# Kernel optimization log

Hardware: AMD Instinct MI355X
Metric: run time of the kernel (lower is better)

## Reference

```python
import jax, jax.numpy as jnp
import numpy as np
from math import factorial

# ---- configuration (init_kwargs: nclasses=40, cfg.bw=16) ----
BW = 16            # spherical bandwidth
NB = 2 * BW        # grid samples per angle
M = 2 * BW - 1     # spectral orders m in [-(BW-1), BW-1]
OFF = BW - 1       # index offset: m -> m + OFF
NCLS = 40
EPS = 1e-5
BATCH = 8

_FACT = [float(factorial(i)) for i in range(4 * BW + 2)]

def _wigner_d(l, beta):
    """Wigner small-d matrix d^l_{m',m}(beta), shape [2l+1, 2l+1]."""
    c, s = np.cos(beta / 2.0), np.sin(beta / 2.0)
    d = np.zeros((2 * l + 1, 2 * l + 1))
    for imp, mp in enumerate(range(-l, l + 1)):
        for im, m in enumerate(range(-l, l + 1)):
            pref = np.sqrt(_FACT[l + mp] * _FACT[l - mp] * _FACT[l + m] * _FACT[l - m])
            acc = 0.0
            for k in range(max(0, m - mp), min(l + m, l - mp) + 1):
                acc += ((-1.0) ** (mp - m + k)
                        / (_FACT[l + m - k] * _FACT[k] * _FACT[l - k - mp] * _FACT[k - m + mp])
                        * c ** (2 * l - 2 * k + m - mp) * s ** (2 * k - m + mp))
            d[imp, im] = pref * acc
    return d

def _build_constants():
    # Driscoll-Healy beta quadrature grid and weights
    betas = np.pi * (2 * np.arange(NB) + 1) / (4 * BW)
    kk = np.arange(BW)
    qw = (2.0 / BW) * np.sin(betas) * (
        np.sin(np.outer(2 * np.arange(NB) + 1, 2 * kk + 1) * np.pi / (4 * BW)) @ (1.0 / (2 * kk + 1)))
    d_beta = np.zeros((NB, BW, M, M))      # d^l_{mn}(beta_j), zero-padded over l
    for j, beta in enumerate(betas):
        for l in range(BW):
            d_beta[j, l, OFF - l:OFF + l + 1, OFF - l:OFF + l + 1] = _wigner_d(l, beta)
    d_eq = np.zeros((BW, M, M))            # d^l_{mn}(pi/2) for the equatorial kernel grid
    for l in range(BW):
        d_eq[l, OFF - l:OFF + l + 1, OFF - l:OFF + l + 1] = _wigner_d(l, np.pi / 2)
    bins = (np.arange(-(BW - 1), BW) % NB).astype(np.int32)  # FFT bin for each order m
    return qw.astype(np.float32), d_beta.astype(np.float32), d_eq.astype(np.float32), bins

_QWn, _DBETAn, _DEQn, _BINSn = _build_constants()
_DBJ = jnp.asarray(_DBETAn)                                   # [NB, L, M, M]
_DEQJ = jnp.asarray(_DEQn)                                    # [L, M, M]
_DEQ0 = jnp.asarray(_DEQn[:, :, OFF])                         # [L, M]  (n = 0 column)
_WD_S2 = jnp.asarray(_QWn[:, None, None] * _DBETAn[:, :, :, OFF])   # [NB, L, M]
_WD_SO3 = jnp.asarray(_QWn[:, None, None, None] * _DBETAn)          # [NB, L, M, M]
_L2 = jnp.asarray((2.0 * np.arange(BW) + 1.0).astype(np.float32))
_BINSJ = jnp.asarray(_BINSn)

def _so3_ifft(z, bias):
    # z: [B, Co, L, M, M] SO(3) spectrum -> real signal [B, Co, NB(beta), NB(alpha), NB(gamma)]
    F = jnp.einsum('bolmn,jlmn,l->bojmn', z, _DBJ, _L2)
    grid = jnp.zeros(F.shape[:3] + (NB, NB), F.dtype)
    grid = grid.at[..., _BINSJ[:, None], _BINSJ[None, :]].set(F)
    sig = jnp.fft.ifft2(grid, axes=(-2, -1)).real * float(NB * NB)
    return sig + bias[None, :, None, None, None]

def _s2_conv(x, W, bias):
    # x: [B, Ci, NB(beta), NB(alpha)]; W: [Ci, Co, NB] kernel on the equatorial grid
    Xf = jnp.fft.fft(x, axis=-1)[..., _BINSJ]                 # [B,Ci,NB,M]
    xh = jnp.einsum('bcjm,jlm->bclm', Xf, _WD_S2)             # S2 FFT -> [B,Ci,L,M]
    Wf = jnp.fft.fft(W, axis=-1)[..., _BINSJ]                 # [Ci,Co,M]
    yh = _DEQ0[:, :, None, None] * jnp.transpose(Wf, (2, 0, 1))[None]   # [L,N,Ci,Co]
    z = jnp.einsum('bilm,lnio->bolmn', xh, jnp.conj(yh))      # S2 correlation -> SO(3) spectrum
    return _so3_ifft(z, bias)

def _so3_conv(x, W, bias):
    # x: [B, Ci, NB(beta), NB(alpha), NB(gamma)]; W: [Ci, Co, NB]
    Xf = jnp.fft.fft2(x, axes=(-2, -1))[..., _BINSJ[:, None], _BINSJ[None, :]]  # [B,Ci,NB,M,M]
    xh = jnp.einsum('bcjmn,jlmn->bclmn', Xf, _WD_SO3)         # SO(3) FFT -> [B,Ci,L,M,M]
    Wf = jnp.fft.fft(W, axis=-1)[..., _BINSJ]                 # [Ci,Co,M]
    yh = _DEQJ[:, :, :, None, None] * jnp.transpose(Wf, (2, 0, 1))[None, :, None]  # [L,N,K,Ci,Co]
    z = jnp.einsum('bilmk,lnkio->bolmn', xh, jnp.conj(yh))    # SO(3) correlation
    return _so3_ifft(z, bias)

def _bn(h, g, b, axes, shape):
    mu = jnp.mean(h, axes, keepdims=True)
    var = jnp.var(h, axes, keepdims=True)
    return (h - mu) * jax.lax.rsqrt(var + EPS) * g.reshape(shape) + b.reshape(shape)

def _forward(x, k1, c1b, bn1_g, bn1_b, k2, c2b, bn2_g, bn2_b, k3, c3b, bn3_g, bn3_b,
             fc1_w, fc1_b, fbn1_g, fbn1_b, fc2_w, fc2_b, fbn2_g, fbn2_b, fc3_w, fc3_b):
    s5 = (1, -1, 1, 1, 1)
    h = _s2_conv(x, k1, c1b)                                  # [B,50,NB,NB,NB]
    h = jax.nn.relu(_bn(h, bn1_g, bn1_b, (0, 2, 3, 4), s5))
    h = _so3_conv(h, k2, c2b)
    h = jax.nn.relu(_bn(h, bn2_g, bn2_b, (0, 2, 3, 4), s5))
    h = _so3_conv(h, k3, c3b)
    h = jax.nn.relu(_bn(h, bn3_g, bn3_b, (0, 2, 3, 4), s5))
    h = h.mean(-1)                                            # integrate over gamma
    h = h.reshape(h.shape[0], h.shape[1], -1).max(-1)         # global max pool -> [B,50]
    h = h @ fc1_w.T + fc1_b
    h = jax.nn.relu(_bn(h, fbn1_g, fbn1_b, (0,), (1, -1)))
    h = h @ fc2_w.T + fc2_b
    h = jax.nn.relu(_bn(h, fbn2_g, fbn2_b, (0,), (1, -1)))
    h = h @ fc3_w.T + fc3_b
    return jax.nn.log_softmax(h, axis=1)

def setup_inputs():
    key = jax.random.key(0)
    ks = jax.random.split(key, 24)
    f32 = jnp.float32
    def kern(k, ci, co):
        return jax.random.normal(k, (ci, co, NB), f32) / np.sqrt(ci * NB).astype(np.float32)
    def lin(k, co, ci):
        return jax.random.normal(k, (co, ci), f32) / np.sqrt(ci).astype(np.float32)
    return {
        'x': jax.random.normal(ks[0], (BATCH, 1, NB, NB), f32),
        'k1': kern(ks[1], 1, 50), 'c1b': 0.01 * jax.random.normal(ks[2], (50,), f32),
        'bn1_g': 1.0 + 0.1 * jax.random.normal(ks[3], (50,), f32),
        'bn1_b': 0.1 * jax.random.normal(ks[4], (50,), f32),
        'k2': kern(ks[5], 50, 50), 'c2b': 0.01 * jax.random.normal(ks[6], (50,), f32),
        'bn2_g': 1.0 + 0.1 * jax.random.normal(ks[7], (50,), f32),
        'bn2_b': 0.1 * jax.random.normal(ks[8], (50,), f32),
        'k3': kern(ks[9], 50, 50), 'c3b': 0.01 * jax.random.normal(ks[10], (50,), f32),
        'bn3_g': 1.0 + 0.1 * jax.random.normal(ks[11], (50,), f32),
        'bn3_b': 0.1 * jax.random.normal(ks[12], (50,), f32),
        'fc1_w': lin(ks[13], 256, 50), 'fc1_b': jnp.zeros((256,), f32),
        'fbn1_g': 1.0 + 0.1 * jax.random.normal(ks[14], (256,), f32),
        'fbn1_b': 0.1 * jax.random.normal(ks[15], (256,), f32),
        'fc2_w': lin(ks[16], 128, 256), 'fc2_b': jnp.zeros((128,), f32),
        'fbn2_g': 1.0 + 0.1 * jax.random.normal(ks[17], (128,), f32),
        'fbn2_b': 0.1 * jax.random.normal(ks[18], (128,), f32),
        'fc3_w': lin(ks[19], NCLS, 128), 'fc3_b': jnp.zeros((NCLS,), f32),
    }

def reference(x, k1, c1b, bn1_g, bn1_b, k2, c2b, bn2_g, bn2_b, k3, c3b, bn3_g, bn3_b,
              fc1_w, fc1_b, fbn1_g, fbn1_b, fc2_w, fc2_b, fbn2_g, fbn2_b, fc3_w, fc3_b):
    return _forward(x, k1, c1b, bn1_g, bn1_b, k2, c2b, bn2_g, bn2_b, k3, c3b, bn3_g, bn3_b,
                    fc1_w, fc1_b, fbn1_g, fbn1_b, fc2_w, fc2_b, fbn2_g, fbn2_b, fc3_w, fc3_b)
```

## Files before the change

### kernel.cpp

```cpp
#include <hip/hip_runtime.h>
#include <math.h>

constexpr int NB = 32;
constexpr int LL = 16;
constexpr int MM = 31;
constexpr int MOFF = 15;
constexpr int NBATCH = 8;
constexpr int NCH = 50;
constexpr int NQ = MM * MM;
constexpr int SPAT = NB * NB * NB;
constexpr long long HN = (long long)NBATCH * NCH * SPAT;

#define PI_D 3.14159265358979323846

__device__ inline float2 c_mk(float x, float y) { float2 r; r.x = x; r.y = y; return r; }

__device__ inline void fill_tw(float2* tw) {
  int t = threadIdx.x;
  if (t < 32) {
    double a = (double)t * (PI_D / 16.0);
    tw[t] = c_mk((float)cos(a), (float)sin(a));
  }
}

__device__ inline int bitrev5(int n) {
  return ((n & 1) << 4) | ((n & 2) << 2) | (n & 4) | ((n & 8) >> 2) | ((n & 16) >> 4);
}

__device__ inline double dpow(double x, int n) {
  double r = 1.0;
  for (int i = 0; i < n; ++i) r *= x;
  return r;
}


__global__ void qw_kernel(float* __restrict__ qw) {
  int j = threadIdx.x;
  if (j >= NB) return;
  double beta = PI_D * (2 * j + 1) / 64.0;
  double acc = 0.0;
  for (int kk = 0; kk < LL; ++kk)
    acc += sin((double)(2 * j + 1) * (2 * kk + 1) * PI_D / 64.0) / (double)(2 * kk + 1);
  qw[j] = (float)((2.0 / 16.0) * sin(beta) * acc);
}

__global__ void wigner_kernel(float* __restrict__ out, int nj, int eqmode) {
  __shared__ double fact[66];
  int tid = threadIdx.x;
  if (tid < 66) { double f = 1.0; for (int i = 2; i <= tid; ++i) f *= (double)i; fact[tid] = f; }
  __syncthreads();
  int total = nj * LL * NQ;
  int idx = blockIdx.x * blockDim.x + tid;
  if (idx >= total) return;
  int q = idx % NQ;
  int l = (idx / NQ) % LL;
  int j = idx / (NQ * LL);
  int mp = q / MM - MOFF;
  int m  = q % MM - MOFF;
  int amp = mp < 0 ? -mp : mp, am = m < 0 ? -m : m;
  float res = 0.f;
  if (amp <= l && am <= l) {
    double beta = eqmode ? (PI_D * 0.5) : (PI_D * (2 * j + 1) / 64.0);
    double c = cos(beta * 0.5), s = sin(beta * 0.5);
    double pref = sqrt(fact[l + mp] * fact[l - mp] * fact[l + m] * fact[l - m]);
    int k0 = max(0, m - mp), k1 = min(l + m, l - mp);
    double acc = 0.0;
    for (int k = k0; k <= k1; ++k) {
      double denom = fact[l + m - k] * fact[k] * fact[l - k - mp] * fact[k - m + mp];
      double term = dpow(c, 2 * l - 2 * k + m - mp) * dpow(s, 2 * k - m + mp) / denom;
      acc += ((mp - m + k) & 1) ? -term : term;
    }
    res = (float)(pref * acc);
  }
  out[idx] = res;
}

__global__ void transpose_d_kernel(const float* __restrict__ dbeta, float* __restrict__ dbT) {
  int idx = blockIdx.x * blockDim.x + threadIdx.x;
  if (idx >= NB * LL * NQ) return;
  int m = idx % MM;
  int n = (idx / MM) % MM;
  int jl = idx / NQ;
  dbT[idx] = dbeta[jl * NQ + m * MM + n];
}


__global__ __launch_bounds__(256) void s2_xh_kernel(const float* __restrict__ x,
                                                    const float* __restrict__ qw,
                                                    const float* __restrict__ dbeta,
                                                    float2* __restrict__ xh1) {
  __shared__ float xt[NB * NB];
  __shared__ float2 Xf0[NB * MM];
  __shared__ float2 tw[32];
  fill_tw(tw);
  int tid = threadIdx.x, b = blockIdx.x;
  for (int e = tid; e < NB * NB; e += 256) xt[e] = x[b * 1024 + e];
  __syncthreads();
  for (int e = tid; e < NB * MM; e += 256) {
    int j = e / MM, mi = e % MM, m = mi - MOFF;
    float re = 0.f, im = 0.f;
    const float* row = xt + j * NB;
    for (int a = 0; a < NB; ++a) {
      float v = row[a];
      float2 t = tw[(m * a) & 31];
      re += v * t.x; im -= v * t.y;
    }
    Xf0[e] = c_mk(re, im);
  }
  __syncthreads();
  for (int e = tid; e < LL * MM; e += 256) {
    int l = e / MM, mi = e % MM;
    float re = 0.f, im = 0.f;
    for (int j = 0; j < NB; ++j) {
      float w = qw[j] * dbeta[(j * LL + l) * NQ + mi * MM + MOFF];
      float2 X = Xf0[j * MM + mi];
      re += w * X.x; im += w * X.y;
    }
    xh1[(b * LL + l) * MM + mi] = c_mk(re, im);
  }
}

__global__ __launch_bounds__(256) void wfft_kernel(const float* __restrict__ W, int CiCo,
                                                   float2* __restrict__ Wf) {
  __shared__ float2 tw[32];
  fill_tw(tw);
  __syncthreads();
  int idx = blockIdx.x * blockDim.x + threadIdx.x;
  if (idx >= MM * CiCo) return;
  int ni = idx / CiCo, ic = idx % CiCo;
  int n = ni - MOFF;
  float re = 0.f, im = 0.f;
  for (int t = 0; t < NB; ++t) {
    float v = W[ic * NB + t];
    float2 tt = tw[(n * t) & 31];
    re += v * tt.x; im -= v * tt.y;
  }
  Wf[idx] = c_mk(re, im);
}

__global__ void s2_z_kernel(const float2* __restrict__ xh1, const float2* __restrict__ Wf1,
                            const float* __restrict__ deq, float2* __restrict__ z) {
  int idx = blockIdx.x * blockDim.x + threadIdx.x;
  if (idx >= NBATCH * NCH * LL * NQ) return;
  int mi = idx % MM; int t = idx / MM;
  int ni = t % MM; t /= MM;
  int l = t % LL; t /= LL;
  int o = t % NCH; int b = t / NCH;
  float d0 = deq[(l * MM + ni) * MM + MOFF];
  float2 xv = xh1[(b * LL + l) * MM + mi];
  float2 wv = Wf1[ni * NCH + o];
  float re = d0 * (xv.x * wv.x + xv.y * wv.y);
  float im = d0 * (xv.y * wv.x - xv.x * wv.y);
  z[idx] = c_mk(re, im);
}


__global__ __launch_bounds__(256) void fjq_kernel(const float2* __restrict__ z,
                                                  const float* __restrict__ dbT,
                                                  float2* __restrict__ F) {
  __shared__ float2 zs[2][LL][8];
  int qg = blockIdx.x % 121;
  int bg = blockIdx.x / 121;
  int tid = threadIdx.x;
  int j = tid >> 3, ql = tid & 7;
  int q = qg * 8 + ql;
  bool qok = q < NQ;
  int qc = qok ? q : NQ - 1;
  float w[LL];
  #pragma unroll
  for (int l = 0; l < LL; ++l)
    w[l] = (2.f * l + 1.f) * dbT[(j * LL + l) * NQ + qc];
  int bo0 = bg * 25;
  if (tid < 128) {
    int l = tid >> 3, qq = qg * 8 + (tid & 7);
    int dd = (qq < NQ) ? (qq / MM - MOFF) : 99; if (dd < 0) dd = -dd;
    zs[0][l][tid & 7] = (l >= dd) ? z[((long long)bo0 * LL + l) * NQ + qq] : c_mk(0.f, 0.f);
  }
  __syncthreads();
  for (int i = 0; i < 25; ++i) {
    int bo = bo0 + i;
    if (i < 24 && tid < 128) {
      int l = tid >> 3, qq = qg * 8 + (tid & 7);
      int dd = (qq < NQ) ? (qq / MM - MOFF) : 99; if (dd < 0) dd = -dd;
      zs[(i + 1) & 1][l][tid & 7] =
          (l >= dd) ? z[((long long)(bo + 1) * LL + l) * NQ + qq] : c_mk(0.f, 0.f);
    }
    float fr = 0.f, fi = 0.f;
    #pragma unroll
    for (int l = 0; l < LL; ++l) {
      float2 zv = zs[i & 1][l][ql];
      fr += w[l] * zv.x; fi += w[l] * zv.y;
    }
    if (qok) F[((long long)bo * NB + j) * NQ + q] = c_mk(fr, fi);
    __syncthreads();
  }
}

__global__ __launch_bounds__(64) void so3_dft_kernel(const float2* __restrict__ F,
                                                     const float* __restrict__ bias,
                                                     float* __restrict__ out,
                                                     float2* __restrict__ parts) {
  __shared__ float Sre[2][32][33];
  __shared__ float Sim[2][32][33];
  __shared__ float2 tw[32];
  fill_tw(tw);
  int tid = threadIdx.x;
  int lane = tid & 31;
  int t = tid >> 5;
  int idx = blockIdx.x * 2 + t;
  int j = idx & 31;
  int bo = idx >> 5;
  int o = bo % NCH;

  Sre[t][16][lane] = 0.f; Sim[t][16][lane] = 0.f;
  Sre[t][lane][16] = 0.f; Sim[t][lane][16] = 0.f;
  __syncthreads();

  const float2* src = F + ((long long)bo * NB + j) * NQ;
  for (int e = lane; e < NQ; e += 32) {
    int ni = e / MM, mi = e % MM;
    float2 v = src[e];
    Sre[t][(ni + 17) & 31][(mi + 17) & 31] = v.x;
    Sim[t][(ni + 17) & 31][(mi + 17) & 31] = v.y;
  }
  __syncthreads();

  float vr[32], vi[32];

  #pragma unroll
  for (int r = 0; r < 32; ++r) { vr[r] = Sre[t][r][lane]; vi[r] = Sim[t][r][lane]; }
  #pragma unroll
  for (int st = 0; st < 5; ++st) {
    const int half = 16 >> st, tmul = 1 << st;
    #pragma unroll
    for (int p = 0; p < 16; ++p) {
      const int j2 = p & (half - 1);
      const int i0 = ((p >> (4 - st)) << (5 - st)) + j2;
      const int i1 = i0 + half;
      float2 tt = tw[(j2 * tmul) & 31];
      float ur = vr[i0], ui = vi[i0], wr = vr[i1], wi = vi[i1];
      float dr = ur - wr, di = ui - wi;
      vr[i0] = ur + wr; vi[i0] = ui + wi;
      vr[i1] = dr * tt.x - di * tt.y;
      vi[i1] = dr * tt.y + di * tt.x;
    }
  }
  #pragma unroll
  for (int k = 0; k < 32; ++k) {
    Sre[t][k][lane] = vr[bitrev5(k)];
    Sim[t][k][lane] = vi[bitrev5(k)];
  }
  __syncthreads();

  #pragma unroll
  for (int m = 0; m < 32; ++m) { vr[m] = Sre[t][lane][m]; vi[m] = Sim[t][lane][m]; }
  #pragma unroll
  for (int st = 0; st < 5; ++st) {
    const int half = 16 >> st, tmul = 1 << st;
    #pragma unroll
    for (int p = 0; p < 16; ++p) {
      const int j2 = p & (half - 1);
      const int i0 = ((p >> (4 - st)) << (5 - st)) + j2;
      const int i1 = i0 + half;
      float2 tt = tw[(j2 * tmul) & 31];
      float ur = vr[i0], ui = vi[i0], wr = vr[i1], wi = vi[i1];
      float dr = ur - wr, di = ui - wi;
      vr[i0] = ur + wr; vi[i0] = ui + wi;
      vr[i1] = dr * tt.x - di * tt.y;
      vi[i1] = dr * tt.y + di * tt.x;
    }
  }

  float bval = bias[o];
  long long obase = (long long)bo * SPAT + (long long)j * 1024 + lane;
  float s1 = 0.f, s2 = 0.f;
  #pragma unroll
  for (int a = 0; a < 32; ++a) {
    float val = vr[bitrev5(a)] + bval;
    out[obase + a * 32] = val;
    s1 += val; s2 += val * val;
  }
  #pragma unroll
  for (int off = 32; off > 0; off >>= 1) {
    s1 += __shfl_down(s1, off);
    s2 += __shfl_down(s2, off);
  }
  if (tid == 0) {
    atomicAdd(&parts[bo].x, s1);
    atomicAdd(&parts[bo].y, s2);
  }
}


__global__ void bn_finalize_kernel(const float2* __restrict__ partials,
                                   const float* __restrict__ g, const float* __restrict__ bb,
                                   float2* __restrict__ sc) {
  int o = threadIdx.x;
  if (o >= NCH) return;
  float s = 0.f, ss = 0.f;
  for (int b = 0; b < NBATCH; ++b) { float2 p = partials[b * NCH + o]; s += p.x; ss += p.y; }
  float inv = 1.f / (float)(NBATCH * SPAT);
  float mu = s * inv;
  float var = ss * inv - mu * mu;
  float scale = g[o] * rsqrtf(var + 1e-5f);
  sc[o] = c_mk(scale, bb[o] - mu * scale);
}


__global__ __launch_bounds__(256) void dft2b_kernel(const float* __restrict__ h,
                                                    const float2* __restrict__ sc,
                                                    float2* __restrict__ Xf) {
  __shared__ float xt[32 * 33];
  __shared__ float2 P[32 * 16];
  __shared__ float2 Xs[NQ];
  __shared__ float2 tw[32];
  fill_tw(tw);
  int tid = threadIdx.x;
  long long blk = blockIdx.x;
  int c = (int)((blk >> 5) % NCH);
  float2 s = sc[c];
  const float* src = h + blk * 1024;
  for (int e = tid; e < 1024; e += 256) {
    float v = src[e];
    xt[(e >> 5) * 33 + (e & 31)] = fmaxf(v * s.x + s.y, 0.f);
  }
  __syncthreads();
  for (int e = tid; e < 512; e += 256) {
    int a = e >> 4, n = e & 15;
    float re = 0.f, im = 0.f;
    const float* row = xt + a * 33;
    #pragma unroll
    for (int g = 0; g < 32; ++g) {
      float v = row[g];
      float2 t = tw[(n * g) & 31];
      re += v * t.x; im -= v * t.y;
    }
    P[a * 16 + n] = c_mk(re, im);
  }
  __syncthreads();
  {
    int e = tid;
    if (e < 256) {
      int mh = e >> 4, n = e & 15;
      float sxx = 0.f, sxy = 0.f, syx = 0.f, syy = 0.f;
      #pragma unroll
      for (int a = 0; a < 32; ++a) {
        float2 p = P[a * 16 + n];
        float2 t = tw[(mh * a) & 31];
        sxx += p.x * t.x; sxy += p.x * t.y;
        syx += p.y * t.x; syy += p.y * t.y;
      }
      float2 Xp = c_mk(sxx + syy, syx - sxy);
      float2 Xm = c_mk(sxx - syy, syx + sxy);
      Xs[(mh + MOFF) * MM + (n + MOFF)] = Xp;
      Xs[(MOFF - mh) * MM + (n + MOFF)] = Xm;
      Xs[(MOFF - mh) * MM + (MOFF - n)] = c_mk(Xp.x, -Xp.y);
      Xs[(mh + MOFF) * MM + (MOFF - n)] = c_mk(Xm.x, -Xm.y);
    }
  }
  __syncthreads();
  float2* dst = Xf + blk * NQ;
  for (int e = tid; e < NQ; e += 256) dst[e] = Xs[e];
}

__global__ void xh_kernel(const float2* __restrict__ Xf, const float* __restrict__ qw,
                          const float* __restrict__ dbeta, float2* __restrict__ xh) {
  int idx = blockIdx.x * blockDim.x + threadIdx.x;
  if (idx >= NBATCH * NCH * NQ) return;
  int q = idx % NQ;
  int bc = idx / NQ;
  int dm = q / MM - MOFF; if (dm < 0) dm = -dm;
  int dn = q % MM - MOFF; if (dn < 0) dn = -dn;
  int lmin = dm > dn ? dm : dn;
  float2 acc[LL];
  #pragma unroll
  for (int l = 0; l < LL; ++l) acc[l] = c_mk(0.f, 0.f);
  for (int j = 0; j < NB; ++j) {
    float2 xv = Xf[((long long)bc * NB + j) * NQ + q];
    float qj = qw[j];
    const float* dbase = dbeta + (long long)(j * LL) * NQ + q;
    #pragma unroll
    for (int l = 0; l < LL; ++l) {
      float w = qj * dbase[l * NQ];
      acc[l].x += w * xv.x;
      acc[l].y += w * xv.y;
    }
  }
  #pragma unroll
  for (int l = 0; l < LL; ++l)
    if (l >= lmin) xh[((long long)bc * LL + l) * NQ + q] = acc[l];
}

__global__ __launch_bounds__(64) void hk_kernel(const float2* __restrict__ xh,
                                                const float* __restrict__ deq,
                                                float2* __restrict__ hk2) {
  int r = blockIdx.x;
  int mi = r % MM;
  int lb = r / MM;
  int b = lb & 7;
  int l = lb >> 3;
  int adm = mi - MOFF; adm = adm < 0 ? -adm : adm;
  if (adm > l) return;
  int ich = threadIdx.x;
  if (ich >= NCH) return;
  float2 row[MM];
  const float2* src = xh + ((long long)(b * NCH + ich) * LL + l) * NQ + mi * MM;
  #pragma unroll
  for (int k = 0; k < MM; ++k) row[k] = src[k];
  const float* dl = deq + l * NQ;
  long long obase = (long long)r * MM * NCH + ich;
  for (int ni = MOFF - l; ni <= MOFF + l; ++ni) {
    const float* dr = dl + ni * MM;
    float re = 0.f, im = 0.f;
    #pragma unroll
    for (int k = 0; k < MM; ++k) {
      float d = dr[k];
      re += d * row[k].x;
      im += d * row[k].y;
    }
    hk2[obase + (long long)ni * NCH] = c_mk(re, im);
  }
}

__global__ __launch_bounds__(256) void z_kernel(const float2* __restrict__ hk2,
                                                const float2* __restrict__ Wf,
                                                float2* __restrict__ z) {
  __shared__ float2 ws[NCH * NCH];
  int blk = blockIdx.x;
  int ni = 0;
  for (;;) {
    int d = ni - MOFF; if (d < 0) d = -d;
    int nt = 32 - 2 * d;
    if (blk < nt) break;
    blk -= nt; ++ni;
  }
  int dmin = ni - MOFF; if (dmin < 0) dmin = -dmin;
  int tid = threadIdx.x;
  {
    const float4* s4 = reinterpret_cast<const float4*>(Wf + ni * (NCH * NCH));
    float4* d4 = reinterpret_cast<float4*>(ws);
    for (int e = tid; e < NCH * NCH / 2; e += 256) d4[e] = s4[e];
  }
  __syncthreads();
  if (tid >= 248) return;
  int r = dmin * 248 + blk * 124 + (tid % 124);
  int o0 = (tid / 124) * 25;
  int mi = r % MM;
  int rem = r / MM;
  int b = rem & 7;
  int l = rem >> 3;

  const float4* h4 = reinterpret_cast<const float4*>(hk2 + ((long long)r * MM + ni) * NCH);

  float2 acc[25];
  #pragma unroll
  for (int u = 0; u < 25; ++u) acc[u] = c_mk(0.f, 0.f);

  for (int ih = 0; ih < 25; ++ih) {
    float4 hv = h4[ih];
    const float2* w0 = ws + (2 * ih) * NCH + o0;
    #pragma unroll
    for (int u = 0; u < 25; ++u) {
      float2 w = w0[u];
      acc[u].x += hv.x * w.x + hv.y * w.y;
      acc[u].y += hv.y * w.x - hv.x * w.y;
    }
    const float2* w1 = w0 + NCH;
    #pragma unroll
    for (int u = 0; u < 25; ++u) {
      float2 w = w1[u];
      acc[u].x += hv.z * w.x + hv.w * w.y;
      acc[u].y += hv.w * w.x - hv.z * w.y;
    }
  }

  long long zbase = (((long long)(b * NCH + o0) * LL + l) * NQ) + ni * MM + mi;
  #pragma unroll
  for (int u = 0; u < 25; ++u)
    z[zbase + (long long)u * LL * NQ] = acc[u];
}


__global__ void pool_kernel(const float* __restrict__ h, const float2* __restrict__ sc,
                            float* __restrict__ pooled) {
  __shared__ float sm[256];
  int tid = threadIdx.x;
  int o = blockIdx.x % NCH;
  float2 s = sc[o];
  const float* base = h + (long long)blockIdx.x * SPAT;
  float best = -1e30f;
  for (int e = tid; e < 1024; e += 256) {
    float acc = 0.f;
    for (int g = 0; g < NB; ++g) {
      float v = base[e * NB + g];
      acc += fmaxf(v * s.x + s.y, 0.f);
    }
    best = fmaxf(best, acc * (1.f / 32.f));
  }
  sm[tid] = best;
  __syncthreads();
  for (int st = 128; st > 0; st >>= 1) {
    if (tid < st) sm[tid] = fmaxf(sm[tid], sm[tid + st]);
    __syncthreads();
  }
  if (tid == 0) pooled[blockIdx.x] = sm[0];
}

__global__ __launch_bounds__(32) void fc1_kernel(const float* __restrict__ pooled,
    const float* __restrict__ fc1w, const float* __restrict__ fc1b,
    const float* __restrict__ g1, const float* __restrict__ b1,
    float* __restrict__ A) {
  int o = blockIdx.x * 32 + threadIdx.x;
  const float* wr = fc1w + o * NCH;
  float v[NBATCH];
  float bias = fc1b[o];
  #pragma unroll
  for (int b = 0; b < NBATCH; ++b) v[b] = bias;
  for (int c = 0; c < NCH; ++c) {
    float w = wr[c];
    #pragma unroll
    for (int b = 0; b < NBATCH; ++b) v[b] += pooled[b * NCH + c] * w;
  }
  float s = 0.f, ss = 0.f;
  #pragma unroll
  for (int b = 0; b < NBATCH; ++b) { s += v[b]; ss += v[b] * v[b]; }
  float mu = s * 0.125f, var = ss * 0.125f - mu * mu;
  float scl = g1[o] * rsqrtf(var + 1e-5f), sh = b1[o] - mu * scl;
  #pragma unroll
  for (int b = 0; b < NBATCH; ++b) A[b * 256 + o] = fmaxf(v[b] * scl + sh, 0.f);
}

__global__ __launch_bounds__(64) void fc2_kernel(const float* __restrict__ A,
    const float* __restrict__ fc2w, const float* __restrict__ fc2b,
    const float* __restrict__ g2, const float* __restrict__ b2,
    float* __restrict__ A2) {
  int tid = threadIdx.x;
  int o = blockIdx.x * 8 + (tid >> 3);
  int b = tid & 7;
  const float4* av = reinterpret_cast<const float4*>(A + b * 256);
  const float4* wv = reinterpret_cast<const float4*>(fc2w + o * 256);
  float acc = fc2b[o];
  #pragma unroll
  for (int c4 = 0; c4 < 64; ++c4) {
    float4 a = av[c4], w = wv[c4];
    acc += a.x * w.x + a.y * w.y + a.z * w.z + a.w * w.w;
  }
  float s = acc, ss = acc * acc;
  #pragma unroll
  for (int m = 1; m < 8; m <<= 1) {
    s += __shfl_xor(s, m);
    ss += __shfl_xor(ss, m);
  }
  float mu = s * 0.125f, var = ss * 0.125f - mu * mu;
  float scl = g2[o] * rsqrtf(var + 1e-5f), sh = b2[o] - mu * scl;
  A2[b * 128 + o] = fmaxf(acc * scl + sh, 0.f);
}

__global__ __launch_bounds__(64) void fc3_kernel(const float* __restrict__ A2,
    const float* __restrict__ fc3w, const float* __restrict__ fc3b,
    float* __restrict__ out) {
  __shared__ float Cm[40];
  int tid = threadIdx.x;
  int b = blockIdx.x;
  if (tid < 40) {
    const float* wr = fc3w + tid * 128;
    const float* ar = A2 + b * 128;
    float acc = fc3b[tid];
    #pragma unroll
    for (int c = 0; c < 128; ++c) acc += ar[c] * wr[c];
    Cm[tid] = acc;
  }
  __syncthreads();
  if (tid == 0) {
    float mx = -1e30f;
    for (int f = 0; f < 40; ++f) mx = fmaxf(mx, Cm[f]);
    float se = 0.f;
    for (int f = 0; f < 40; ++f) se += expf(Cm[f] - mx);
    float lse = mx + logf(se);
    for (int f = 0; f < 40; ++f) out[b * 40 + f] = Cm[f] - lse;
  }
}


extern "C" void kernel_launch(void* const* d_in, const int* in_sizes, int n_in,
                              void* d_out, int out_size, void* d_ws, size_t ws_size,
                              hipStream_t stream) {
  (void)in_sizes; (void)n_in; (void)out_size;
  const float* x    = (const float*)d_in[0];
  const float* k1   = (const float*)d_in[1];
  const float* c1b  = (const float*)d_in[2];
  const float* bn1g = (const float*)d_in[3];
  const float* bn1b = (const float*)d_in[4];
  const float* k2   = (const float*)d_in[5];
  const float* c2b  = (const float*)d_in[6];
  const float* bn2g = (const float*)d_in[7];
  const float* bn2b = (const float*)d_in[8];
  const float* k3   = (const float*)d_in[9];
  const float* c3b  = (const float*)d_in[10];
  const float* bn3g = (const float*)d_in[11];
  const float* bn3b = (const float*)d_in[12];
  const float* fc1w = (const float*)d_in[13];
  const float* fc1b = (const float*)d_in[14];
  const float* g1   = (const float*)d_in[15];
  const float* bb1  = (const float*)d_in[16];
  const float* fc2w = (const float*)d_in[17];
  const float* fc2b = (const float*)d_in[18];
  const float* g2   = (const float*)d_in[19];
  const float* bb2  = (const float*)d_in[20];
  const float* fc3w = (const float*)d_in[21];
  const float* fc3b = (const float*)d_in[22];
  float* out = (float*)d_out;

  char* ws = (char*)d_ws;
  size_t off = 0;
  auto alloc = [&](size_t n) -> char* {
    char* p = ws + off;
    off += (n + 255) & ~(size_t)255;
    return p;
  };

  float*  dbeta  = (float*)alloc(sizeof(float) * NB * LL * NQ);
  float*  dbT    = (float*)alloc(sizeof(float) * NB * LL * NQ);
  float*  deq    = (float*)alloc(sizeof(float) * LL * NQ);
  float*  qw     = (float*)alloc(sizeof(float) * NB);
  float2* xh1    = (float2*)alloc(sizeof(float2) * NBATCH * LL * MM);
  float2* Wf     = (float2*)alloc(sizeof(float2) * MM * NCH * NCH);
  float2* parts  = (float2*)alloc(sizeof(float2) * NBATCH * NCH);
  float2* bnsc   = (float2*)alloc(sizeof(float2) * 64);
  float*  pooled = (float*)alloc(sizeof(float) * NBATCH * NCH);
  float*  Abuf   = (float*)alloc(sizeof(float) * NBATCH * 256);
  float*  A2buf  = (float*)alloc(sizeof(float) * NBATCH * 128);
  float*  HA     = (float*)alloc(sizeof(float) * (size_t)HN);
  float*  HB     = (float*)alloc(sizeof(float) * (size_t)HN);
  size_t XFB = (size_t)NBATCH * NCH * NB * NQ * sizeof(float2);
  size_t XHB = (size_t)NBATCH * NCH * LL * NQ * sizeof(float2);
  char* AR = alloc(XFB + XHB);
  float2* Xf  = (float2*)AR;
  float2* xh  = (float2*)(AR + XFB);
  float2* hk2 = (float2*)AR;
  float2* zb  = (float2*)(AR + XFB);
  float2* Fb  = (float2*)AR;

  if (ws_size < off) return;

  const int T = 256;
  const size_t PARTS_B = sizeof(float2) * NBATCH * NCH;
  qw_kernel<<<1, 32, 0, stream>>>(qw);
  wigner_kernel<<<(NB * LL * NQ + T - 1) / T, T, 0, stream>>>(dbeta, NB, 0);
  wigner_kernel<<<(LL * NQ + T - 1) / T, T, 0, stream>>>(deq, 1, 1);
  transpose_d_kernel<<<(NB * LL * NQ + T - 1) / T, T, 0, stream>>>(dbeta, dbT);

  s2_xh_kernel<<<NBATCH, T, 0, stream>>>(x, qw, dbeta, xh1);
  wfft_kernel<<<(MM * 1 * NCH + T - 1) / T, T, 0, stream>>>(k1, 1 * NCH, Wf);
  s2_z_kernel<<<(NBATCH * NCH * LL * NQ + T - 1) / T, T, 0, stream>>>(xh1, Wf, deq, zb);
  fjq_kernel<<<121 * 16, T, 0, stream>>>(zb, dbT, Fb);
  hipMemsetAsync(parts, 0, PARTS_B, stream);
  so3_dft_kernel<<<NBATCH * NCH * NB / 2, 64, 0, stream>>>(Fb, c1b, HA, parts);
  bn_finalize_kernel<<<1, 64, 0, stream>>>(parts, bn1g, bn1b, bnsc);

  dft2b_kernel<<<NBATCH * NCH * NB, T, 0, stream>>>(HA, bnsc, Xf);
  xh_kernel<<<(NBATCH * NCH * NQ + T - 1) / T, T, 0, stream>>>(Xf, qw, dbeta, xh);
  wfft_kernel<<<(MM * NCH * NCH + T - 1) / T, T, 0, stream>>>(k2, NCH * NCH, Wf);
  hk_kernel<<<NBATCH * LL * MM, 64, 0, stream>>>(xh, deq, hk2);
  z_kernel<<<512, T, 0, stream>>>(hk2, Wf, zb);
  fjq_kernel<<<121 * 16, T, 0, stream>>>(zb, dbT, Fb);
  hipMemsetAsync(parts, 0, PARTS_B, stream);
  so3_dft_kernel<<<NBATCH * NCH * NB / 2, 64, 0, stream>>>(Fb, c2b, HB, parts);
  bn_finalize_kernel<<<1, 64, 0, stream>>>(parts, bn2g, bn2b, bnsc);

  dft2b_kernel<<<NBATCH * NCH * NB, T, 0, stream>>>(HB, bnsc, Xf);
  xh_kernel<<<(NBATCH * NCH * NQ + T - 1) / T, T, 0, stream>>>(Xf, qw, dbeta, xh);
  wfft_kernel<<<(MM * NCH * NCH + T - 1) / T, T, 0, stream>>>(k3, NCH * NCH, Wf);
  hk_kernel<<<NBATCH * LL * MM, 64, 0, stream>>>(xh, deq, hk2);
  z_kernel<<<512, T, 0, stream>>>(hk2, Wf, zb);
  fjq_kernel<<<121 * 16, T, 0, stream>>>(zb, dbT, Fb);
  hipMemsetAsync(parts, 0, PARTS_B, stream);
  so3_dft_kernel<<<NBATCH * NCH * NB / 2, 64, 0, stream>>>(Fb, c3b, HA, parts);
  bn_finalize_kernel<<<1, 64, 0, stream>>>(parts, bn3g, bn3b, bnsc);

  pool_kernel<<<NBATCH * NCH, T, 0, stream>>>(HA, bnsc, pooled);
  fc1_kernel<<<8, 32, 0, stream>>>(pooled, fc1w, fc1b, g1, bb1, Abuf);
  fc2_kernel<<<16, 64, 0, stream>>>(Abuf, fc2w, fc2b, g2, bb2, A2buf);
  fc3_kernel<<<8, 64, 0, stream>>>(A2buf, fc3w, fc3b, out);
}
```

Measured before the change: 761.5 us.

## Replace direct 2D DFT with register radix-2 FFT per 32x32 slice

Replaces the shared-memory direct O(N^2) two-stage DFT over each 32x32 slice with a per-thread 32-point radix-2 FFT held in registers. One thread handles one row, then one column after a shared-memory transpose, and two slices share a 64-thread block. The goal is to cut the arithmetic and shared-memory traffic of the direct DFT. The cost is high register use (64 floats per thread) and smaller blocks, and the output writes are strided by MM across lanes. It assumes bitrev5 is already defined elsewhere in the file.

```diff
diff --git a/kernel.cpp b/kernel.cpp
--- a/kernel.cpp
+++ b/kernel.cpp
@@ -307,60 +307,82 @@
 }
 
 
-__global__ __launch_bounds__(256) void dft2b_kernel(const float* __restrict__ h,
-                                                    const float2* __restrict__ sc,
-                                                    float2* __restrict__ Xf) {
-  __shared__ float xt[32 * 33];
-  __shared__ float2 P[32 * 16];
-  __shared__ float2 Xs[NQ];
+__global__ __launch_bounds__(64) void dft2f_kernel(const float* __restrict__ h,
+                                                   const float2* __restrict__ sc,
+                                                   float2* __restrict__ Xf) {
+  __shared__ float Sre[2][32][33];
+  __shared__ float Sim[2][32][33];
   __shared__ float2 tw[32];
   fill_tw(tw);
   int tid = threadIdx.x;
-  long long blk = blockIdx.x;
-  int c = (int)((blk >> 5) % NCH);
+  int lane = tid & 31;
+  int t = tid >> 5;
+  long long idx = blockIdx.x * 2 + t;
+  int c = (int)((idx >> 5) % NCH);
   float2 s = sc[c];
-  const float* src = h + blk * 1024;
-  for (int e = tid; e < 1024; e += 256) {
+
+  const float* src = h + idx * 1024;
+  for (int e = lane; e < 1024; e += 32) {
     float v = src[e];
-    xt[(e >> 5) * 33 + (e & 31)] = fmaxf(v * s.x + s.y, 0.f);
-  }
-  __syncthreads();
-  for (int e = tid; e < 512; e += 256) {
-    int a = e >> 4, n = e & 15;
-    float re = 0.f, im = 0.f;
-    const float* row = xt + a * 33;
-    #pragma unroll
-    for (int g = 0; g < 32; ++g) {
-      float v = row[g];
-      float2 t = tw[(n * g) & 31];
-      re += v * t.x; im -= v * t.y;
-    }
-    P[a * 16 + n] = c_mk(re, im);
-  }
-  __syncthreads();
-  {
-    int e = tid;
-    if (e < 256) {
-      int mh = e >> 4, n = e & 15;
-      float sxx = 0.f, sxy = 0.f, syx = 0.f, syy = 0.f;
-      #pragma unroll
-      for (int a = 0; a < 32; ++a) {
-        float2 p = P[a * 16 + n];
-        float2 t = tw[(mh * a) & 31];
-        sxx += p.x * t.x; sxy += p.x * t.y;
-        syx += p.y * t.x; syy += p.y * t.y;
-      }
-      float2 Xp = c_mk(sxx + syy, syx - sxy);
-      float2 Xm = c_mk(sxx - syy, syx + sxy);
-      Xs[(mh + MOFF) * MM + (n + MOFF)] = Xp;
-      Xs[(MOFF - mh) * MM + (n + MOFF)] = Xm;
-      Xs[(MOFF - mh) * MM + (MOFF - n)] = c_mk(Xp.x, -Xp.y);
-      Xs[(mh + MOFF) * MM + (MOFF - n)] = c_mk(Xm.x, -Xm.y);
-    }
-  }
-  __syncthreads();
-  float2* dst = Xf + blk * NQ;
-  for (int e = tid; e < NQ; e += 256) dst[e] = Xs[e];
+    Sre[t][e >> 5][e & 31] = fmaxf(v * s.x + s.y, 0.f);
+  }
+  __syncthreads();
+
+  float vr[32], vi[32];
+
+  #pragma unroll
+  for (int g = 0; g < 32; ++g) { vr[g] = Sre[t][lane][g]; vi[g] = 0.f; }
+  #pragma unroll
+  for (int st = 0; st < 5; ++st) {
+    const int half = 16 >> st, tmul = 1 << st;
+    #pragma unroll
+    for (int p = 0; p < 16; ++p) {
+      const int j2 = p & (half - 1);
+      const int i0 = ((p >> (4 - st)) << (5 - st)) + j2;
+      const int i1 = i0 + half;
+      float2 tt = tw[(j2 * tmul) & 31];
+      float ur = vr[i0], ui = vi[i0], wr = vr[i1], wi = vi[i1];
+      float dr = ur - wr, di = ui - wi;
+      vr[i0] = ur + wr; vi[i0] = ui + wi;
+      vr[i1] = dr * tt.x + di * tt.y;
+      vi[i1] = di * tt.x - dr * tt.y;
+    }
+  }
+  #pragma unroll
+  for (int k = 0; k < 32; ++k) {
+    Sre[t][k][lane] = vr[bitrev5(k)];
+    Sim[t][k][lane] = vi[bitrev5(k)];
+  }
+  __syncthreads();
+
+  #pragma unroll
+  for (int a = 0; a < 32; ++a) { vr[a] = Sre[t][lane][a]; vi[a] = Sim[t][lane][a]; }
+  #pragma unroll
+  for (int st = 0; st < 5; ++st) {
+    const int half = 16 >> st, tmul = 1 << st;
+    #pragma unroll
+    for (int p = 0; p < 16; ++p) {
+      const int j2 = p & (half - 1);
+      const int i0 = ((p >> (4 - st)) << (5 - st)) + j2;
+      const int i1 = i0 + half;
+      float2 tt = tw[(j2 * tmul) & 31];
+      float ur = vr[i0], ui = vi[i0], wr = vr[i1], wi = vi[i1];
+      float dr = ur - wr, di = ui - wi;
+      vr[i0] = ur + wr; vi[i0] = ui + wi;
+      vr[i1] = dr * tt.x + di * tt.y;
+      vi[i1] = di * tt.x - dr * tt.y;
+    }
+  }
+
+  int ni = (lane + 15) & 31;
+  if (ni < MM) {
+    float2* dst = Xf + idx * NQ + ni;
+    #pragma unroll
+    for (int mi = 0; mi < MM; ++mi) {
+      const int km = (mi + 17) & 31;
+      dst[mi * MM] = c_mk(vr[bitrev5(km)], vi[bitrev5(km)]);
+    }
+  }
 }
 
 __global__ void xh_kernel(const float2* __restrict__ Xf, const float* __restrict__ qw,
@@ -658,7 +680,7 @@
   so3_dft_kernel<<<NBATCH * NCH * NB / 2, 64, 0, stream>>>(Fb, c1b, HA, parts);
   bn_finalize_kernel<<<1, 64, 0, stream>>>(parts, bn1g, bn1b, bnsc);
 
-  dft2b_kernel<<<NBATCH * NCH * NB, T, 0, stream>>>(HA, bnsc, Xf);
+  dft2f_kernel<<<NBATCH * NCH * NB / 2, 64, 0, stream>>>(HA, bnsc, Xf);
   xh_kernel<<<(NBATCH * NCH * NQ + T - 1) / T, T, 0, stream>>>(Xf, qw, dbeta, xh);
   wfft_kernel<<<(MM * NCH * NCH + T - 1) / T, T, 0, stream>>>(k2, NCH * NCH, Wf);
   hk_kernel<<<NBATCH * LL * MM, 64, 0, stream>>>(xh, deq, hk2);
@@ -668,7 +690,7 @@
   so3_dft_kernel<<<NBATCH * NCH * NB / 2, 64, 0, stream>>>(Fb, c2b, HB, parts);
   bn_finalize_kernel<<<1, 64, 0, stream>>>(parts, bn2g, bn2b, bnsc);
 
-  dft2b_kernel<<<NBATCH * NCH * NB, T, 0, stream>>>(HB, bnsc, Xf);
+  dft2f_kernel<<<NBATCH * NCH * NB / 2, 64, 0, stream>>>(HB, bnsc, Xf);
   xh_kernel<<<(NBATCH * NCH * NQ + T - 1) / T, T, 0, stream>>>(Xf, qw, dbeta, xh);
   wfft_kernel<<<(MM * NCH * NCH + T - 1) / T, T, 0, stream>>>(k3, NCH * NCH, Wf);
   hk_kernel<<<NBATCH * LL * MM, 64, 0, stream>>>(xh, deq, hk2);
```

Result: faster. 709.9 us (-6.8%).
